# Performance work log

Measured on AMD Instinct MI355X. Metric: run time of the kernel, lower is better.

The kernel has to match this reference:

```python
import jax, jax.numpy as jnp
import numpy as np

N, E, C, H, D = 50000, 800000, 128, 8, 16  # nodes, edges, in_channels, heads, out_channels
EDIM, SDIM = 18, 64                         # edge_dim, seq_bias_dim
HID_S = H * 16                              # seq_bias_processor hidden = heads*16 = 128

def setup_inputs() -> dict:
    key = jax.random.key(0)
    ks = jax.random.split(key, 24)
    s = 0.05
    f32 = jnp.float32
    inp = {
        "x": jax.random.normal(ks[0], (N, C), f32),
        "edge_index": jax.random.randint(ks[1], (2, E), 0, N),
        "edge_attr": jax.random.uniform(ks[2], (E, EDIM), f32),
        "seq_features": jax.random.normal(ks[3], (N, SDIM), f32),
        # LayerNorm
        "ln_g": jnp.ones((C,), f32),
        "ln_b": jnp.zeros((C,), f32),
        # Q/K/V projections (torch Linear weights: [out, in])
        "Wq": jax.random.normal(ks[4], (H * D, C), f32) * s, "bq": jnp.zeros((H * D,), f32),
        "Wk": jax.random.normal(ks[5], (H * D, C), f32) * s, "bk": jnp.zeros((H * D,), f32),
        "Wv": jax.random.normal(ks[6], (H * D, C), f32) * s, "bv": jnp.zeros((H * D,), f32),
        # edge_type_encoders[0]: Linear(16,32) -> ReLU -> Linear(32,8)
        "We0a": jax.random.normal(ks[7], (32, EDIM - 2), f32) * s, "be0a": jnp.zeros((32,), f32),
        "We0b": jax.random.normal(ks[8], (H, 32), f32) * s, "be0b": jnp.zeros((H,), f32),
        # edge_type_encoders[1]
        "We1a": jax.random.normal(ks[9], (32, EDIM - 2), f32) * s, "be1a": jnp.zeros((32,), f32),
        "We1b": jax.random.normal(ks[10], (H, 32), f32) * s, "be1b": jnp.zeros((H,), f32),
        # seq_bias_processor: Linear(64,128) -> GELU -> Linear(128,8) -> Tanh
        "Ws1": jax.random.normal(ks[11], (HID_S, SDIM), f32) * s, "bs1": jnp.zeros((HID_S,), f32),
        "Ws2": jax.random.normal(ks[12], (H, HID_S), f32) * s, "bs2": jnp.zeros((H,), f32),
    }
    return inp

def reference(x, edge_index, edge_attr, seq_features,
              ln_g, ln_b, Wq, bq, Wk, bk, Wv, bv,
              We0a, be0a, We0b, be0b, We1a, be1a, We1b, be1b,
              Ws1, bs1, Ws2, bs2):
    src, dst = edge_index[0], edge_index[1]  # PyG: message i=dst (target), j=src (source)
    identity = x
    # LayerNorm (eps=1e-5, biased variance)
    mu = x.mean(-1, keepdims=True)
    var = x.var(-1, keepdims=True)
    h = (x - mu) * jax.lax.rsqrt(var + 1e-5) * ln_g + ln_b
    # Q/K/V [N, H, D]
    q = (h @ Wq.T + bq).reshape(N, H, D)
    k = (h @ Wk.T + bk).reshape(N, H, D)
    v = (h @ Wv.T + bv).reshape(N, H, D)
    # per-edge attention logits [E, H]
    logits = (q[dst] * k[src]).sum(-1) / jnp.sqrt(jnp.float32(D))
    # edge-type conditional modifier
    ef = edge_attr[:, :-2]
    etype = jnp.argmax(edge_attr[:, -2:], axis=-1)
    m0 = jax.nn.relu(ef @ We0a.T + be0a) @ We0b.T + be0b
    m1 = jax.nn.relu(ef @ We1a.T + be1a) @ We1b.T + be1b
    logits = logits + jnp.where((etype == 0)[:, None], m0, m1)
    # sequence-based bias: normalize, diff, MLP with GELU + Tanh, scaled by 0.1
    sn = seq_features / jnp.maximum(jnp.linalg.norm(seq_features, axis=-1, keepdims=True), 1e-12)
    sd = sn[dst] - sn[src]
    sb = jnp.tanh(jax.nn.gelu(sd @ Ws1.T + bs1, approximate=False) @ Ws2.T + bs2)
    logits = logits + 0.1 * sb  # temperature = 1.0
    # grouped (scatter) stable softmax over destination nodes
    mx = jax.ops.segment_max(logits, dst, num_segments=N)
    ex = jnp.exp(logits - mx[dst])
    sm = jax.ops.segment_sum(ex, dst, num_segments=N)
    w = ex / (sm[dst] + 1e-12)
    # weighted message + scatter-add aggregation (concat heads)
    msg = v[src] * w[:, :, None]
    out = jax.ops.segment_sum(msg, dst, num_segments=N).reshape(N, H * D)
    out = jax.nn.gelu(out, approximate=False)  # torch nn.GELU default = exact erf
    return out + identity
```

## Files before the change

### kernel.cpp

```cpp
#include <hip/hip_runtime.h>
#include <hip/hip_fp16.h>

#define NN 50000
#define EE 800000
#define NCHUNK 784

typedef unsigned int u32;
typedef unsigned short u16;
typedef _Float16 f16x8 __attribute__((ext_vector_type(8)));
typedef float f32x4 __attribute__((ext_vector_type(4)));

__device__ __forceinline__ float bf_lo(u32 u){ return __uint_as_float(u << 16); }
__device__ __forceinline__ float bf_hi(u32 u){ return __uint_as_float(u & 0xffff0000u); }
__device__ __forceinline__ u16 f2bf(float f){
  u32 x = __float_as_uint(f);
  x += 0x7fffu + ((x >> 16) & 1u);
  return (u16)(x >> 16);
}
__device__ __forceinline__ float gelu_exact(float x){
  return x * 0.5f * (1.0f + erff(x * 0.70710678118654752f));
}
__device__ __forceinline__ float rcp_fast(float x){ return __builtin_amdgcn_rcpf(x); }
__device__ __forceinline__ float gelu_fast(float x){
  float x2 = x * x;
  float y  = x * fmaf(x2, 0.0356774081f, 0.7978845608f);
  float e  = __expf(y + y);
  return x - x * rcp_fast(e + 1.0f);
}
__device__ __forceinline__ float tanh_fast(float x){
  float e = __expf(x + x);
  return 1.0f - 2.0f * rcp_fast(e + 1.0f);
}
__device__ __forceinline__ int atomic_inc_i32(int* p){
  return __hip_atomic_fetch_add(p, 1, __ATOMIC_RELAXED, __HIP_MEMORY_SCOPE_AGENT);
}
__device__ __forceinline__ __half2 as_h2(u32 u){ return __builtin_bit_cast(__half2, u); }
__device__ __forceinline__ u32 pack2f(float a, float b){
  __half2 h = __floats2half2_rn(a, b);
  return __builtin_bit_cast(u32, h);
}
__device__ __forceinline__ float h2_lo(__half2 h){ return __half2float(__low2half(h)); }
__device__ __forceinline__ float h2_hi(__half2 h){ return __half2float(__high2half(h)); }

union FragU { uint4 u; f16x8 v; };

__global__ __launch_bounds__(256) void count_k(const int* __restrict__ ei, int* __restrict__ deg)
{
  int e = blockIdx.x * 256 + threadIdx.x;
  atomic_inc_i32(&deg[ei[EE + e]]);
}

__global__ __launch_bounds__(256) void chunksum_k(const int* __restrict__ deg, int* __restrict__ csum)
{
  const int c = blockIdx.x * 4 + (threadIdx.x >> 6);
  const int lane = threadIdx.x & 63;
  const int idx = c * 64 + lane;
  int v = (idx < NN) ? deg[idx] : 0;
  #pragma unroll
  for (int o = 1; o < 64; o <<= 1) v += __shfl_xor(v, o);
  if (lane == 0) csum[c] = v;
}

__global__ __launch_bounds__(64) void chunkscan_k(const int* __restrict__ csum, int* __restrict__ cbase)
{
  const int lane = threadIdx.x;
  const int CH = 13;
  const int base = lane * CH;
  int s = 0;
  #pragma unroll
  for (int j = 0; j < CH; j++) {
    int c = base + j;
    s += (c < NCHUNK) ? csum[c] : 0;
  }
  int inc = s;
  #pragma unroll
  for (int off = 1; off < 64; off <<= 1) {
    int v = __shfl_up(inc, off);
    if (lane >= off) inc += v;
  }
  int run = inc - s;
  #pragma unroll
  for (int j = 0; j < CH; j++) {
    int c = base + j;
    if (c < NCHUNK) {
      cbase[c] = run;
      run += csum[c];
    }
  }
}

__global__ __launch_bounds__(256) void writeoffs_k(
    const int* __restrict__ deg, const int* __restrict__ cbase,
    int* __restrict__ offs, int* __restrict__ cursor)
{
  const int c = blockIdx.x * 4 + (threadIdx.x >> 6);
  const int lane = threadIdx.x & 63;
  const int idx = c * 64 + lane;
  int d = (idx < NN) ? deg[idx] : 0;
  int inc = d;
  #pragma unroll
  for (int off = 1; off < 64; off <<= 1) {
    int v = __shfl_up(inc, off);
    if (lane >= off) inc += v;
  }
  int off_ = cbase[c] + inc - d;
  if (idx < NN) {
    offs[idx] = off_;
    cursor[idx] = off_;
  }
}

__global__ __launch_bounds__(256) void scatter_pairs_k(
    const int* __restrict__ ei, int* __restrict__ cursor,
    int* __restrict__ psrc, int* __restrict__ pe)
{
  int e = blockIdx.x * 256 + threadIdx.x;
  int dst = ei[EE + e];
  int pos = atomic_inc_i32(&cursor[dst]);
  psrc[pos] = ei[e];
  pe[pos]   = e;
}

__global__ __launch_bounds__(512) void node_pre(
    const float* __restrict__ x, const float* __restrict__ seq,
    const float* __restrict__ ln_g, const float* __restrict__ ln_b,
    const float* __restrict__ Wq, const float* __restrict__ bq,
    const float* __restrict__ Wk, const float* __restrict__ bk,
    const float* __restrict__ Wv, const float* __restrict__ bv,
    __half* __restrict__ qb, __half* __restrict__ kb,
    u16* __restrict__ vb, __half* __restrict__ snb)
{
  __shared__ __align__(16) u16 h16[64][136];
  const int t = threadIdx.x;
  const int nbase = blockIdx.x * 64;

  {
    const int row = t >> 3, sub = t & 7;
    const int n = nbase + row;
    if (n < NN) {
      const float* xp = x + (size_t)n * 128 + sub * 16;
      float vals[16];
      float s = 0.f, ss = 0.f;
      #pragma unroll
      for (int j = 0; j < 16; j += 4) {
        float4 v4 = *(const float4*)(xp + j);
        vals[j] = v4.x; vals[j+1] = v4.y; vals[j+2] = v4.z; vals[j+3] = v4.w;
        s += v4.x + v4.y + v4.z + v4.w;
        ss += v4.x*v4.x + v4.y*v4.y + v4.z*v4.z + v4.w*v4.w;
      }
      #pragma unroll
      for (int o = 1; o < 8; o <<= 1) { s += __shfl_xor(s, o); ss += __shfl_xor(ss, o); }
      float mu = s * (1.f / 128.f);
      float var = ss * (1.f / 128.f) - mu * mu;
      float rs = rsqrtf(var + 1e-5f);
      #pragma unroll
      for (int j = 0; j < 16; j += 2) {
        int c = sub * 16 + j;
        float v0 = (vals[j]   - mu) * rs * ln_g[c]   + ln_b[c];
        float v1 = (vals[j+1] - mu) * rs * ln_g[c+1] + ln_b[c+1];
        *(u32*)&h16[row][c] = pack2f(v0, v1);
      }
      const float* sp = seq + (size_t)n * 64 + sub * 8;
      float4 a = *(const float4*)(sp);
      float4 b4 = *(const float4*)(sp + 4);
      float q2 = a.x*a.x + a.y*a.y + a.z*a.z + a.w*a.w
               + b4.x*b4.x + b4.y*b4.y + b4.z*b4.z + b4.w*b4.w;
      #pragma unroll
      for (int o = 1; o < 8; o <<= 1) q2 += __shfl_xor(q2, o);
      float inv = 1.0f / fmaxf(sqrtf(q2), 1e-12f);
      __half* op = snb + (size_t)n * 64 + sub * 8;
      op[0]=__float2half(a.x*inv);  op[1]=__float2half(a.y*inv);
      op[2]=__float2half(a.z*inv);  op[3]=__float2half(a.w*inv);
      op[4]=__float2half(b4.x*inv); op[5]=__float2half(b4.y*inv);
      op[6]=__float2half(b4.z*inv); op[7]=__float2half(b4.w*inv);
    }
  }

  const int lane = t & 63, wid = t >> 6;
  const int lr = lane & 15;
  const int lk = lane >> 4;
  const int tile0 = wid * 3;

  FragU Bf[3][4];
  float bias[3];
  #pragma unroll
  for (int ti = 0; ti < 3; ti++) {
    int tile = tile0 + ti;
    int mat = tile >> 3;
    int colm = (tile & 7) * 16 + lr;
    const float* W = (mat == 0) ? Wq : (mat == 1) ? Wk : Wv;
    const float* B = (mat == 0) ? bq : (mat == 1) ? bk : bv;
    bias[ti] = B[colm];
    const float* wrow = W + (size_t)colm * 128;
    #pragma unroll
    for (int ks = 0; ks < 4; ks++) {
      const float* wp = wrow + ks * 32 + lk * 8;
      float4 wa = *(const float4*)(wp);
      float4 wb = *(const float4*)(wp + 4);
      Bf[ti][ks].u.x = pack2f(wa.x, wa.y);
      Bf[ti][ks].u.y = pack2f(wa.z, wa.w);
      Bf[ti][ks].u.z = pack2f(wb.x, wb.y);
      Bf[ti][ks].u.w = pack2f(wb.z, wb.w);
    }
  }
  __syncthreads();

  #pragma unroll
  for (int mt = 0; mt < 4; mt++) {
    FragU A[4];
    #pragma unroll
    for (int ks = 0; ks < 4; ks++)
      A[ks].u = *(const uint4*)&h16[mt * 16 + lr][ks * 32 + lk * 8];
    #pragma unroll
    for (int ti = 0; ti < 3; ti++) {
      f32x4 acc = { bias[ti], bias[ti], bias[ti], bias[ti] };
      #pragma unroll
      for (int ks = 0; ks < 4; ks++)
        acc = __builtin_amdgcn_mfma_f32_16x16x32_f16(A[ks].v, Bf[ti][ks].v, acc, 0, 0, 0);
      int tile = tile0 + ti;
      int mat = tile >> 3;
      int colm = (tile & 7) * 16 + lr;
      __half* Oh = (mat == 0) ? qb : kb;
      #pragma unroll
      for (int r = 0; r < 4; r++) {
        int node = nbase + mt * 16 + lk * 4 + r;
        if (node < NN) {
          float val = acc[r];
          if (mat == 2) vb[(size_t)node * 128 + colm] = f2bf(val);
          else          Oh[(size_t)node * 128 + colm] = __float2half(val);
        }
      }
    }
  }
}

__global__ __launch_bounds__(256, 4) void edge_fused(
    const int* __restrict__ ei, const float* __restrict__ edge_attr,
    const __half* __restrict__ qb, const __half* __restrict__ kb,
    const __half* __restrict__ snb,
    const float* __restrict__ We0a, const float* __restrict__ be0a,
    const float* __restrict__ We0b, const float* __restrict__ be0b,
    const float* __restrict__ We1a, const float* __restrict__ be1a,
    const float* __restrict__ We1b, const float* __restrict__ be1b,
    const float* __restrict__ Ws1, const float* __restrict__ bs1,
    const float* __restrict__ Ws2, const float* __restrict__ bs2,
    uint4* __restrict__ exw)
{
  __shared__ __align__(16) u16 h1lds[4][16][136];
  __shared__ __align__(16) uint4 sWs1F[1024];
  __shared__ __align__(16) uint4 sWs2F[128];
  __shared__ u32   sWeah[2 * 264];
  __shared__ u32   sWebTh[2 * 136];
  __shared__ float sbea[64];
  __shared__ float sbeb[16];

  const int t = threadIdx.x;
  const int lane = t & 63, wid = t >> 6;
  const int lr = lane & 15;
  const int lk = lane >> 4;
  const int ebase = blockIdx.x * 256 + wid * 64;

  for (int idx = t; idx < 512; idx += 256) {
    int e2 = idx >> 8, rem = idx & 255, j = rem >> 3, q = rem & 7;
    const float* W = e2 ? We1a : We0a;
    sWeah[e2 * 264 + rem] = pack2f(W[j * 16 + 2 * q], W[j * 16 + 2 * q + 1]);
  }
  {
    int e2 = t >> 7, rem = t & 127, j = rem >> 2, q = rem & 3;
    const float* W = e2 ? We1b : We0b;
    sWebTh[e2 * 136 + rem] = pack2f(W[(2 * q) * 32 + j], W[(2 * q + 1) * 32 + j]);
  }
  if (t < 64) sbea[t] = (t < 32) ? be0a[t] : be1a[t - 32];
  if (t < 16) sbeb[t] = (t < 8) ? be0b[t] : be1b[t - 8];

  for (int fid = t; fid < 1024; fid += 256) {
    int lf = fid & 63, tk = (fid >> 6) & 1, jt = fid >> 7;
    int lrf = lf & 15, lkf = lf >> 4;
    const float* wp = Ws1 + (size_t)(jt * 16 + lrf) * 64 + tk * 32 + lkf * 8;
    float4 wa = *(const float4*)(wp);
    float4 wb = *(const float4*)(wp + 4);
    uint4 fr;
    fr.x = pack2f(wa.x, wa.y); fr.y = pack2f(wa.z, wa.w);
    fr.z = pack2f(wb.x, wb.y); fr.w = pack2f(wb.z, wb.w);
    sWs1F[fid] = fr;
  }
  if (t < 128) {
    int lrf = t & 7, lkf = (t >> 3) & 3, tk = t >> 5;
    const float* wp = Ws2 + (size_t)lrf * 128 + tk * 32 + lkf * 8;
    float4 wa = *(const float4*)(wp);
    float4 wb = *(const float4*)(wp + 4);
    uint4 fr;
    fr.x = pack2f(wa.x, wa.y); fr.y = pack2f(wa.z, wa.w);
    fr.z = pack2f(wb.x, wb.y); fr.w = pack2f(wb.z, wb.w);
    sWs2F[t] = fr;
  }

  float b1v[8];
  #pragma unroll
  for (int jt = 0; jt < 8; jt++) b1v[jt] = bs1[jt * 16 + lr];
  const float b2v = (lr < 8) ? bs2[lr] : 0.f;

  const int srcR = ei[ebase + lane];
  const int dstR = ei[EE + ebase + lane];
  const char* snbB = (const char*)snb;

  __syncthreads();

  float sbreg[16];
  #pragma unroll
  for (int g = 0; g < 4; g++) {
    const int d_e = __shfl(dstR, g * 16 + lr);
    const int s_e = __shfl(srcR, g * 16 + lr);
    FragU A0, A1;
    {
      uint4 ua = *(const uint4*)(snbB + (size_t)d_e * 128 + 0 * 64 + lk * 16);
      uint4 ub = *(const uint4*)(snbB + (size_t)s_e * 128 + 0 * 64 + lk * 16);
      A0.u.x = __builtin_bit_cast(u32, __hsub2(as_h2(ua.x), as_h2(ub.x)));
      A0.u.y = __builtin_bit_cast(u32, __hsub2(as_h2(ua.y), as_h2(ub.y)));
      A0.u.z = __builtin_bit_cast(u32, __hsub2(as_h2(ua.z), as_h2(ub.z)));
      A0.u.w = __builtin_bit_cast(u32, __hsub2(as_h2(ua.w), as_h2(ub.w)));
      uint4 uc = *(const uint4*)(snbB + (size_t)d_e * 128 + 1 * 64 + lk * 16);
      uint4 ud = *(const uint4*)(snbB + (size_t)s_e * 128 + 1 * 64 + lk * 16);
      A1.u.x = __builtin_bit_cast(u32, __hsub2(as_h2(uc.x), as_h2(ud.x)));
      A1.u.y = __builtin_bit_cast(u32, __hsub2(as_h2(uc.y), as_h2(ud.y)));
      A1.u.z = __builtin_bit_cast(u32, __hsub2(as_h2(uc.z), as_h2(ud.z)));
      A1.u.w = __builtin_bit_cast(u32, __hsub2(as_h2(uc.w), as_h2(ud.w)));
    }
    #pragma unroll
    for (int jt = 0; jt < 8; jt++) {
      FragU Bf0, Bf1;
      Bf0.u = sWs1F[(jt * 2 + 0) * 64 + lane];
      Bf1.u = sWs1F[(jt * 2 + 1) * 64 + lane];
      f32x4 acc = { b1v[jt], b1v[jt], b1v[jt], b1v[jt] };
      acc = __builtin_amdgcn_mfma_f32_16x16x32_f16(A0.v, Bf0.v, acc, 0, 0, 0);
      acc = __builtin_amdgcn_mfma_f32_16x16x32_f16(A1.v, Bf1.v, acc, 0, 0, 0);
      #pragma unroll
      for (int r = 0; r < 4; r++) {
        float gg = gelu_fast(acc[r]);
        h1lds[wid][lk * 4 + r][jt * 16 + lr] = __builtin_bit_cast(u16, (_Float16)gg);
      }
    }
    f32x4 acc2 = { b2v, b2v, b2v, b2v };
    #pragma unroll
    for (int tk = 0; tk < 4; tk++) {
      FragU A2, B2f;
      A2.u = *(const uint4*)&h1lds[wid][lr][tk * 32 + lk * 8];
      if (lr < 8) B2f.u = sWs2F[tk * 32 + lk * 8 + lr];
      else        B2f.u = make_uint4(0, 0, 0, 0);
      acc2 = __builtin_amdgcn_mfma_f32_16x16x32_f16(A2.v, B2f.v, acc2, 0, 0, 0);
    }
    #pragma unroll
    for (int r = 0; r < 4; r++) sbreg[g * 4 + r] = acc2[r];
  }

  u16* sbuf = &h1lds[wid][0][0];
  if (lr < 8) {
    #pragma unroll
    for (int g = 0; g < 4; g++)
      #pragma unroll
      for (int r = 0; r < 4; r++)
        sbuf[(g * 16 + lk * 4 + r) * 8 + lr] =
            __builtin_bit_cast(u16, (_Float16)sbreg[g * 4 + r]);
  }

  const int e = ebase + lane;
  const int src = srcR;
  const int dst = dstR;

  __half2 ef2[8]; float a16, a17;
  {
    const float2* p2 = (const float2*)(edge_attr + (size_t)e * 18);
    float2 p[9];
    #pragma unroll
    for (int i = 0; i < 9; i++) p[i] = p2[i];
    #pragma unroll
    for (int i = 0; i < 8; i++) ef2[i] = __floats2half2_rn(p[i].x, p[i].y);
    a16 = p[8].x; a17 = p[8].y;
  }
  const int sel = (a17 > a16) ? 1 : 0;
  const u32* Wah = sWeah + sel * 264;
  const u32* Wbh = sWebTh + sel * 136;
  const float* ba = sbea + sel * 32;
  const float* bb = sbeb + sel * 8;

  __half2 m2[4];
  #pragma unroll
  for (int q = 0; q < 4; q++) m2[q] = __floats2half2_rn(bb[2 * q], bb[2 * q + 1]);
  for (int j = 0; j < 32; j++) {
    __half2 a = __floats2half2_rn(0.f, 0.f);
    #pragma unroll
    for (int q = 0; q < 8; q++) a = __hfma2(as_h2(Wah[j * 8 + q]), ef2[q], a);
    float hs = h2_lo(a) + h2_hi(a) + ba[j];
    hs = fmaxf(hs, 0.f);
    __half2 hs2 = __float2half2_rn(hs);
    #pragma unroll
    for (int q = 0; q < 4; q++) m2[q] = __hfma2(as_h2(Wbh[j * 4 + q]), hs2, m2[q]);
  }
  float m[8];
  #pragma unroll
  for (int q = 0; q < 4; q++) { m[2*q] = h2_lo(m2[q]); m[2*q+1] = h2_hi(m2[q]); }

  float tv[8];
  {
    uint4 sb4 = ((const uint4*)sbuf)[lane];
    u32 wv[4] = {sb4.x, sb4.y, sb4.z, sb4.w};
    #pragma unroll
    for (int q = 0; q < 4; q++) {
      tv[2*q]   = tanh_fast(h2_lo(as_h2(wv[q])));
      tv[2*q+1] = tanh_fast(h2_hi(as_h2(wv[q])));
    }
  }

  {
    const uint4* qp4 = (const uint4*)(qb + (size_t)dst * 128);
    const uint4* kp4 = (const uint4*)(kb + (size_t)src * 128);
    float ex[8];
    #pragma unroll
    for (int h = 0; h < 8; h++) {
      uint4 qa = qp4[2*h], qc = qp4[2*h+1];
      uint4 ka = kp4[2*h], kc = kp4[2*h+1];
      __half2 d2 = __floats2half2_rn(0.f, 0.f);
      d2 = __hfma2(as_h2(qa.x), as_h2(ka.x), d2);
      d2 = __hfma2(as_h2(qa.y), as_h2(ka.y), d2);
      d2 = __hfma2(as_h2(qa.z), as_h2(ka.z), d2);
      d2 = __hfma2(as_h2(qa.w), as_h2(ka.w), d2);
      d2 = __hfma2(as_h2(qc.x), as_h2(kc.x), d2);
      d2 = __hfma2(as_h2(qc.y), as_h2(kc.y), d2);
      d2 = __hfma2(as_h2(qc.z), as_h2(kc.z), d2);
      d2 = __hfma2(as_h2(qc.w), as_h2(kc.w), d2);
      float dot = h2_lo(d2) + h2_hi(d2);
      float logit = dot * 0.25f + m[h] + 0.1f * tv[h];
      ex[h] = __expf(logit);
    }
    uint4 st;
    st.x = (u32)f2bf(ex[0]) | ((u32)f2bf(ex[1]) << 16);
    st.y = (u32)f2bf(ex[2]) | ((u32)f2bf(ex[3]) << 16);
    st.z = (u32)f2bf(ex[4]) | ((u32)f2bf(ex[5]) << 16);
    st.w = (u32)f2bf(ex[6]) | ((u32)f2bf(ex[7]) << 16);
    exw[e] = st;
  }
}

__global__ __launch_bounds__(256) void aggregate_k(
    const int* __restrict__ offs, const int* __restrict__ deg,
    const int* __restrict__ psrc, const int* __restrict__ pe,
    const u32* __restrict__ exw, const u32* __restrict__ vb32,
    const float* __restrict__ x, float* __restrict__ out)
{
  const int n = (blockIdx.x * 256 + threadIdx.x) >> 6;
  const int lane = threadIdx.x & 63;
  if (n >= NN) return;
  const int s = offs[n];
  const int end = s + deg[n];
  const int word  = lane >> 4;
  const int shift = ((lane >> 3) & 1) << 4;

  float s0 = 0.f, s1 = 0.f, dn = 0.f;
  int i = s;
  for (; i + 4 <= end; i += 4) {
    int e0 = pe[i], e1 = pe[i+1], e2 = pe[i+2], e3 = pe[i+3];
    int p0 = psrc[i], p1 = psrc[i+1], p2 = psrc[i+2], p3 = psrc[i+3];
    u32 k0 = exw[(size_t)e0 * 4 + word];
    u32 k1 = exw[(size_t)e1 * 4 + word];
    u32 k2 = exw[(size_t)e2 * 4 + word];
    u32 k3 = exw[(size_t)e3 * 4 + word];
    u32 v0 = vb32[(size_t)p0 * 64 + lane];
    u32 v1 = vb32[(size_t)p1 * 64 + lane];
    u32 v2 = vb32[(size_t)p2 * 64 + lane];
    u32 v3 = vb32[(size_t)p3 * 64 + lane];
    float x0 = __uint_as_float(((k0 >> shift) & 0xffffu) << 16);
    float x1 = __uint_as_float(((k1 >> shift) & 0xffffu) << 16);
    float x2 = __uint_as_float(((k2 >> shift) & 0xffffu) << 16);
    float x3 = __uint_as_float(((k3 >> shift) & 0xffffu) << 16);
    s0 = fmaf(bf_lo(v0), x0, s0); s1 = fmaf(bf_hi(v0), x0, s1); dn += x0;
    s0 = fmaf(bf_lo(v1), x1, s0); s1 = fmaf(bf_hi(v1), x1, s1); dn += x1;
    s0 = fmaf(bf_lo(v2), x2, s0); s1 = fmaf(bf_hi(v2), x2, s1); dn += x2;
    s0 = fmaf(bf_lo(v3), x3, s0); s1 = fmaf(bf_hi(v3), x3, s1); dn += x3;
  }
  for (; i < end; i++) {
    int ee = pe[i];
    int sp = psrc[i];
    u32 pkv = exw[(size_t)ee * 4 + word];
    float ex = __uint_as_float(((pkv >> shift) & 0xffffu) << 16);
    u32 vv = vb32[(size_t)sp * 64 + lane];
    s0 = fmaf(bf_lo(vv), ex, s0);
    s1 = fmaf(bf_hi(vv), ex, s1);
    dn += ex;
  }
  float inv = 1.0f / (dn + 1e-12f);
  float2 xx = *(const float2*)(x + (size_t)n * 128 + lane * 2);
  float2 o;
  o.x = gelu_exact(s0 * inv) + xx.x;
  o.y = gelu_exact(s1 * inv) + xx.y;
  *(float2*)(out + (size_t)n * 128 + lane * 2) = o;
}

extern "C" void kernel_launch(void* const* d_in, const int* in_sizes, int n_in,
                              void* d_out, int out_size, void* d_ws, size_t ws_size,
                              hipStream_t stream)
{
  const float* x    = (const float*)d_in[0];
  const int*   ei   = (const int*)d_in[1];
  const float* ea   = (const float*)d_in[2];
  const float* seq  = (const float*)d_in[3];
  const float* ln_g = (const float*)d_in[4];
  const float* ln_b = (const float*)d_in[5];
  const float* Wq   = (const float*)d_in[6];
  const float* bq   = (const float*)d_in[7];
  const float* Wk   = (const float*)d_in[8];
  const float* bk   = (const float*)d_in[9];
  const float* Wv   = (const float*)d_in[10];
  const float* bv   = (const float*)d_in[11];
  const float* We0a = (const float*)d_in[12];
  const float* be0a = (const float*)d_in[13];
  const float* We0b = (const float*)d_in[14];
  const float* be0b = (const float*)d_in[15];
  const float* We1a = (const float*)d_in[16];
  const float* be1a = (const float*)d_in[17];
  const float* We1b = (const float*)d_in[18];
  const float* be1b = (const float*)d_in[19];
  const float* Ws1  = (const float*)d_in[20];
  const float* bs1  = (const float*)d_in[21];
  const float* Ws2  = (const float*)d_in[22];
  const float* bs2  = (const float*)d_in[23];
  float* out = (float*)d_out;

  char* w = (char*)d_ws;
  __half* qb   = (__half*)w;                       w += (size_t)NN * 128 * 2;
  __half* kb   = (__half*)w;                       w += (size_t)NN * 128 * 2;
  u16*    vb   = (u16*)w;                          w += (size_t)NN * 128 * 2;
  __half* snb  = (__half*)w;                       w += (size_t)NN * 64 * 2;
  uint4*  exw  = (uint4*)w;                        w += (size_t)EE * 16;
  int*    psrc = (int*)w;                          w += (size_t)EE * 4;
  int*    pe   = (int*)w;                          w += (size_t)EE * 4;
  int*    deg  = (int*)w;                          w += (size_t)NN * 4;
  int*    offs = (int*)w;                          w += (size_t)NN * 4;
  int*    cursor = (int*)w;                        w += (size_t)NN * 4;
  int*    csum = (int*)w;                          w += (size_t)NCHUNK * 4;
  int*    cbase = (int*)w;                         w += (size_t)NCHUNK * 4;

  (void)hipMemsetAsync(psrc, 0, (size_t)EE * 4 * 2 + (size_t)NN * 4, stream);

  count_k<<<EE / 256, 256, 0, stream>>>(ei, deg);
  chunksum_k<<<NCHUNK / 4, 256, 0, stream>>>(deg, csum);
  chunkscan_k<<<1, 64, 0, stream>>>(csum, cbase);
  writeoffs_k<<<NCHUNK / 4, 256, 0, stream>>>(deg, cbase, offs, cursor);
  scatter_pairs_k<<<EE / 256, 256, 0, stream>>>(ei, cursor, psrc, pe);

  node_pre<<<(NN + 63) / 64, 512, 0, stream>>>(
      x, seq, ln_g, ln_b, Wq, bq, Wk, bk, Wv, bv, qb, kb, vb, snb);

  edge_fused<<<EE / 256, 256, 0, stream>>>(
      ei, ea, qb, kb, snb,
      We0a, be0a, We0b, be0b, We1a, be1a, We1b, be1b,
      Ws1, bs1, Ws2, bs2, exw);

  aggregate_k<<<(NN * 64) / 256, 256, 0, stream>>>(
      offs, deg, psrc, pe, (const u32*)exw, (const u32*)vb, x, out);
}
```

Measured before the change: 334.1 us.

## Write edge weights in CSR order, shrink edge kernel LDS, raise occupancy

The scatter kernel now records each edge's CSR position (rank), and edge_fused writes its packed exp weights straight to that sorted slot. Aggregation can then read exw contiguously instead of doing an indirect gather through pe. Ws1 fragments are packed once by a new small kernel and read from global/L2 instead of being staged in LDS by every block. The hidden-layer LDS buffer is halved by splitting the MLP into two halves, which allows launch bounds of 8 blocks; the cost is scattered 16-byte writes in the edge kernel and uncached repeated global fragment loads.

```diff
diff --git a/kernel.cpp b/kernel.cpp
--- a/kernel.cpp
+++ b/kernel.cpp
@@ -112,13 +112,30 @@
 
 __global__ __launch_bounds__(256) void scatter_pairs_k(
     const int* __restrict__ ei, int* __restrict__ cursor,
-    int* __restrict__ psrc, int* __restrict__ pe)
+    int* __restrict__ psrc, int* __restrict__ rank)
 {
   int e = blockIdx.x * 256 + threadIdx.x;
   int dst = ei[EE + e];
   int pos = atomic_inc_i32(&cursor[dst]);
   psrc[pos] = ei[e];
-  pe[pos]   = e;
+  rank[e] = pos;
+}
+
+__global__ __launch_bounds__(256) void prep_frags(
+    const float* __restrict__ Ws1, uint4* __restrict__ W1F)
+{
+  int fid = blockIdx.x * 256 + threadIdx.x;
+  if (fid < 1024) {
+    int lf = fid & 63, tk = (fid >> 6) & 1, jt = fid >> 7;
+    int lrf = lf & 15, lkf = lf >> 4;
+    const float* wp = Ws1 + (size_t)(jt * 16 + lrf) * 64 + tk * 32 + lkf * 8;
+    float4 wa = *(const float4*)(wp);
+    float4 wb = *(const float4*)(wp + 4);
+    uint4 fr;
+    fr.x = pack2f(wa.x, wa.y); fr.y = pack2f(wa.z, wa.w);
+    fr.z = pack2f(wb.x, wb.y); fr.w = pack2f(wb.z, wb.w);
+    W1F[fid] = fr;
+  }
 }
 
 __global__ __launch_bounds__(512) void node_pre(
@@ -234,20 +251,20 @@
   }
 }
 
-__global__ __launch_bounds__(256, 4) void edge_fused(
+__global__ __launch_bounds__(256, 8) void edge_fused(
     const int* __restrict__ ei, const float* __restrict__ edge_attr,
     const __half* __restrict__ qb, const __half* __restrict__ kb,
-    const __half* __restrict__ snb,
+    const __half* __restrict__ snb, const uint4* __restrict__ W1F,
+    const int* __restrict__ rank,
     const float* __restrict__ We0a, const float* __restrict__ be0a,
     const float* __restrict__ We0b, const float* __restrict__ be0b,
     const float* __restrict__ We1a, const float* __restrict__ be1a,
     const float* __restrict__ We1b, const float* __restrict__ be1b,
-    const float* __restrict__ Ws1, const float* __restrict__ bs1,
+    const float* __restrict__ bs1,
     const float* __restrict__ Ws2, const float* __restrict__ bs2,
     uint4* __restrict__ exw)
 {
-  __shared__ __align__(16) u16 h1lds[4][16][136];
-  __shared__ __align__(16) uint4 sWs1F[1024];
+  __shared__ __align__(16) u16 h1lds[4][16][72];
   __shared__ __align__(16) uint4 sWs2F[128];
   __shared__ u32   sWeah[2 * 264];
   __shared__ u32   sWebTh[2 * 136];
@@ -272,18 +289,6 @@
   }
   if (t < 64) sbea[t] = (t < 32) ? be0a[t] : be1a[t - 32];
   if (t < 16) sbeb[t] = (t < 8) ? be0b[t] : be1b[t - 8];
-
-  for (int fid = t; fid < 1024; fid += 256) {
-    int lf = fid & 63, tk = (fid >> 6) & 1, jt = fid >> 7;
-    int lrf = lf & 15, lkf = lf >> 4;
-    const float* wp = Ws1 + (size_t)(jt * 16 + lrf) * 64 + tk * 32 + lkf * 8;
-    float4 wa = *(const float4*)(wp);
-    float4 wb = *(const float4*)(wp + 4);
-    uint4 fr;
-    fr.x = pack2f(wa.x, wa.y); fr.y = pack2f(wa.z, wa.w);
-    fr.z = pack2f(wb.x, wb.y); fr.w = pack2f(wb.z, wb.w);
-    sWs1F[fid] = fr;
-  }
   if (t < 128) {
     int lrf = t & 7, lkf = (t >> 3) & 3, tk = t >> 5;
     const float* wp = Ws2 + (size_t)lrf * 128 + tk * 32 + lkf * 8;
@@ -302,6 +307,7 @@
 
   const int srcR = ei[ebase + lane];
   const int dstR = ei[EE + ebase + lane];
+  const int re   = rank[ebase + lane];
   const char* snbB = (const char*)snb;
 
   __syncthreads();
@@ -326,11 +332,12 @@
       A1.u.z = __builtin_bit_cast(u32, __hsub2(as_h2(uc.z), as_h2(ud.z)));
       A1.u.w = __builtin_bit_cast(u32, __hsub2(as_h2(uc.w), as_h2(ud.w)));
     }
-    #pragma unroll
-    for (int jt = 0; jt < 8; jt++) {
+    f32x4 acc2 = { b2v, b2v, b2v, b2v };
+    #pragma unroll
+    for (int jt = 0; jt < 4; jt++) {
       FragU Bf0, Bf1;
-      Bf0.u = sWs1F[(jt * 2 + 0) * 64 + lane];
-      Bf1.u = sWs1F[(jt * 2 + 1) * 64 + lane];
+      Bf0.u = W1F[(jt * 2 + 0) * 64 + lane];
+      Bf1.u = W1F[(jt * 2 + 1) * 64 + lane];
       f32x4 acc = { b1v[jt], b1v[jt], b1v[jt], b1v[jt] };
       acc = __builtin_amdgcn_mfma_f32_16x16x32_f16(A0.v, Bf0.v, acc, 0, 0, 0);
       acc = __builtin_amdgcn_mfma_f32_16x16x32_f16(A1.v, Bf1.v, acc, 0, 0, 0);
@@ -340,11 +347,32 @@
         h1lds[wid][lk * 4 + r][jt * 16 + lr] = __builtin_bit_cast(u16, (_Float16)gg);
       }
     }
-    f32x4 acc2 = { b2v, b2v, b2v, b2v };
-    #pragma unroll
-    for (int tk = 0; tk < 4; tk++) {
+    #pragma unroll
+    for (int tk = 0; tk < 2; tk++) {
       FragU A2, B2f;
       A2.u = *(const uint4*)&h1lds[wid][lr][tk * 32 + lk * 8];
+      if (lr < 8) B2f.u = sWs2F[tk * 32 + lk * 8 + lr];
+      else        B2f.u = make_uint4(0, 0, 0, 0);
+      acc2 = __builtin_amdgcn_mfma_f32_16x16x32_f16(A2.v, B2f.v, acc2, 0, 0, 0);
+    }
+    #pragma unroll
+    for (int jt = 4; jt < 8; jt++) {
+      FragU Bf0, Bf1;
+      Bf0.u = W1F[(jt * 2 + 0) * 64 + lane];
+      Bf1.u = W1F[(jt * 2 + 1) * 64 + lane];
+      f32x4 acc = { b1v[jt], b1v[jt], b1v[jt], b1v[jt] };
+      acc = __builtin_amdgcn_mfma_f32_16x16x32_f16(A0.v, Bf0.v, acc, 0, 0, 0);
+      acc = __builtin_amdgcn_mfma_f32_16x16x32_f16(A1.v, Bf1.v, acc, 0, 0, 0);
+      #pragma unroll
+      for (int r = 0; r < 4; r++) {
+        float gg = gelu_fast(acc[r]);
+        h1lds[wid][lk * 4 + r][(jt - 4) * 16 + lr] = __builtin_bit_cast(u16, (_Float16)gg);
+      }
+    }
+    #pragma unroll
+    for (int tk = 2; tk < 4; tk++) {
+      FragU A2, B2f;
+      A2.u = *(const uint4*)&h1lds[wid][lr][(tk - 2) * 32 + lk * 8];
       if (lr < 8) B2f.u = sWs2F[tk * 32 + lk * 8 + lr];
       else        B2f.u = make_uint4(0, 0, 0, 0);
       acc2 = __builtin_amdgcn_mfma_f32_16x16x32_f16(A2.v, B2f.v, acc2, 0, 0, 0);
@@ -437,15 +465,15 @@
     st.y = (u32)f2bf(ex[2]) | ((u32)f2bf(ex[3]) << 16);
     st.z = (u32)f2bf(ex[4]) | ((u32)f2bf(ex[5]) << 16);
     st.w = (u32)f2bf(ex[6]) | ((u32)f2bf(ex[7]) << 16);
-    exw[e] = st;
+    exw[re] = st;
   }
 }
 
 __global__ __launch_bounds__(256) void aggregate_k(
     const int* __restrict__ offs, const int* __restrict__ deg,
-    const int* __restrict__ psrc, const int* __restrict__ pe,
-    const u32* __restrict__ exw, const u32* __restrict__ vb32,
-    const float* __restrict__ x, float* __restrict__ out)
+    const int* __restrict__ psrc, const u32* __restrict__ exw,
+    const u32* __restrict__ vb32, const float* __restrict__ x,
+    float* __restrict__ out)
 {
   const int n = (blockIdx.x * 256 + threadIdx.x) >> 6;
   const int lane = threadIdx.x & 63;
@@ -458,12 +486,11 @@
   float s0 = 0.f, s1 = 0.f, dn = 0.f;
   int i = s;
   for (; i + 4 <= end; i += 4) {
-    int e0 = pe[i], e1 = pe[i+1], e2 = pe[i+2], e3 = pe[i+3];
     int p0 = psrc[i], p1 = psrc[i+1], p2 = psrc[i+2], p3 = psrc[i+3];
-    u32 k0 = exw[(size_t)e0 * 4 + word];
-    u32 k1 = exw[(size_t)e1 * 4 + word];
-    u32 k2 = exw[(size_t)e2 * 4 + word];
-    u32 k3 = exw[(size_t)e3 * 4 + word];
+    u32 k0 = exw[(size_t)(i  ) * 4 + word];
+    u32 k1 = exw[(size_t)(i+1) * 4 + word];
+    u32 k2 = exw[(size_t)(i+2) * 4 + word];
+    u32 k3 = exw[(size_t)(i+3) * 4 + word];
     u32 v0 = vb32[(size_t)p0 * 64 + lane];
     u32 v1 = vb32[(size_t)p1 * 64 + lane];
     u32 v2 = vb32[(size_t)p2 * 64 + lane];
@@ -478,9 +505,8 @@
     s0 = fmaf(bf_lo(v3), x3, s0); s1 = fmaf(bf_hi(v3), x3, s1); dn += x3;
   }
   for (; i < end; i++) {
-    int ee = pe[i];
     int sp = psrc[i];
-    u32 pkv = exw[(size_t)ee * 4 + word];
+    u32 pkv = exw[(size_t)i * 4 + word];
     float ex = __uint_as_float(((pkv >> shift) & 0xffffu) << 16);
     u32 vv = vb32[(size_t)sp * 64 + lane];
     s0 = fmaf(bf_lo(vv), ex, s0);
@@ -532,29 +558,31 @@
   __half* snb  = (__half*)w;                       w += (size_t)NN * 64 * 2;
   uint4*  exw  = (uint4*)w;                        w += (size_t)EE * 16;
   int*    psrc = (int*)w;                          w += (size_t)EE * 4;
-  int*    pe   = (int*)w;                          w += (size_t)EE * 4;
+  int*    rank = (int*)w;                          w += (size_t)EE * 4;
   int*    deg  = (int*)w;                          w += (size_t)NN * 4;
   int*    offs = (int*)w;                          w += (size_t)NN * 4;
   int*    cursor = (int*)w;                        w += (size_t)NN * 4;
   int*    csum = (int*)w;                          w += (size_t)NCHUNK * 4;
   int*    cbase = (int*)w;                         w += (size_t)NCHUNK * 4;
-
-  (void)hipMemsetAsync(psrc, 0, (size_t)EE * 4 * 2 + (size_t)NN * 4, stream);
+  uint4*  W1F  = (uint4*)w;                        w += (size_t)1024 * 16;
+
+  (void)hipMemsetAsync(deg, 0, (size_t)NN * 4, stream);
 
   count_k<<<EE / 256, 256, 0, stream>>>(ei, deg);
   chunksum_k<<<NCHUNK / 4, 256, 0, stream>>>(deg, csum);
   chunkscan_k<<<1, 64, 0, stream>>>(csum, cbase);
   writeoffs_k<<<NCHUNK / 4, 256, 0, stream>>>(deg, cbase, offs, cursor);
-  scatter_pairs_k<<<EE / 256, 256, 0, stream>>>(ei, cursor, psrc, pe);
+  scatter_pairs_k<<<EE / 256, 256, 0, stream>>>(ei, cursor, psrc, rank);
+  prep_frags<<<4, 256, 0, stream>>>(Ws1, W1F);
 
   node_pre<<<(NN + 63) / 64, 512, 0, stream>>>(
       x, seq, ln_g, ln_b, Wq, bq, Wk, bk, Wv, bv, qb, kb, vb, snb);
 
   edge_fused<<<EE / 256, 256, 0, stream>>>(
-      ei, ea, qb, kb, snb,
+      ei, ea, qb, kb, snb, W1F, rank,
       We0a, be0a, We0b, be0b, We1a, be1a, We1b, be1b,
-      Ws1, bs1, Ws2, bs2, exw);
+      bs1, Ws2, bs2, exw);
 
   aggregate_k<<<(NN * 64) / 256, 256, 0, stream>>>(
-      offs, deg, psrc, pe, (const u32*)exw, (const u32*)vb, x, out);
-}
+      offs, deg, psrc, (const u32*)exw, (const u32*)vb, x, out);
+}
```

Result: slower. 453.2 us (+35.6%).
